# Kernel tuning notes

Measured on AMD Instinct MI355X. Metric: run time of the kernel, lower is better.

The kernel has to match this reference:

```python
import jax, jax.numpy as jnp
import numpy as np

N, E, D, H, C = 50000, 1600000, 256, 8, 32

def setup_inputs() -> dict:
    key = jax.random.key(0)
    ks = jax.random.split(key, 7)
    feat = jax.random.normal(ks[0], (N, D), dtype=jnp.float32)
    edge_weight = jax.random.uniform(ks[1], (E,), dtype=jnp.float32)
    W_lin = jax.random.normal(ks[2], (D, H * C), dtype=jnp.float32) * (1.0 / np.sqrt(D))
    att_l = jax.random.normal(ks[3], (1, H, C), dtype=jnp.float32) * (1.0 / np.sqrt(H))
    att_r = jax.random.normal(ks[4], (1, H, C), dtype=jnp.float32) * (1.0 / np.sqrt(H))
    W_res = jax.random.normal(ks[5], (D, H * C), dtype=jnp.float32) * (1.0 / np.sqrt(D))
    edge_index = jax.random.randint(ks[6], (2, E), 0, N, dtype=jnp.int32)
    return {"feat": feat, "edge_weight": edge_weight, "W_lin": W_lin,
            "att_l": att_l, "att_r": att_r, "W_res": W_res, "edge_index": edge_index}

def reference(feat, edge_weight, W_lin, att_l, att_r, W_res, edge_index):
    n_nodes = feat.shape[0]
    h, c = att_l.shape[1], att_l.shape[2]
    src, dst = edge_index[0], edge_index[1]
    # node projection: [N, H, C]
    x = (feat @ W_lin).reshape(n_nodes, h, c)
    alpha_l = (x * att_l).sum(-1)  # [N, H]
    alpha_r = (x * att_r).sum(-1)  # [N, H]
    # per-edge scores [E, H]
    alpha = alpha_l[src] + alpha_r[dst]
    alpha = edge_weight[:, None] * alpha
    alpha = jnp.where(alpha > 0, alpha, 0.2 * alpha)  # leaky_relu(0.2)
    # segment softmax over destination nodes
    amax = jax.lax.stop_gradient(jax.ops.segment_max(alpha, dst, num_segments=n_nodes))
    ex = jnp.exp(alpha - amax[dst])
    denom = jax.ops.segment_sum(ex, dst, num_segments=n_nodes)
    coeff = ex / (denom[dst] + 1e-16)  # [E, H]
    # weighted message aggregation
    msg = x[src] * coeff[:, :, None]  # [E, H, C]
    agg = jax.ops.segment_sum(msg, dst, num_segments=n_nodes)  # [N, H, C]
    out = jax.nn.elu(agg).reshape(n_nodes, h * c)
    out = out + feat @ W_res  # residual
    return out
```

## Files before the change

kernel.cpp:

```cpp
#include <hip/hip_runtime.h>
#include <stdint.h>

#define D_DIM 256
#define NPAD  640

typedef __bf16 bf16x8 __attribute__((ext_vector_type(8)));
typedef float  f32x4  __attribute__((ext_vector_type(4)));

__device__ __forceinline__ float bf2f(unsigned short u) {
  union { unsigned int i; float f; } cv; cv.i = ((unsigned int)u) << 16; return cv.f;
}
__device__ __forceinline__ unsigned short f2bf(float f) {
  union { float f; unsigned int i; } cv; cv.f = f;
  unsigned int i = cv.i;
  unsigned int lsb = (i >> 16) & 1u;
  i += 0x7fffu + lsb;
  return (unsigned short)(i >> 16);
}
__device__ __forceinline__ void gld16(const void* gptr, void* lptr) {
  __builtin_amdgcn_global_load_lds(
      (const __attribute__((address_space(1))) unsigned int*)gptr,
      (__attribute__((address_space(3))) unsigned int*)lptr, 16, 0, 0);
}

__global__ __launch_bounds__(256) void setup_fused(
    const float* __restrict__ feat, unsigned short* __restrict__ fb,
    const float* __restrict__ W_lin, const float* __restrict__ W_res,
    const float* __restrict__ att_l, const float* __restrict__ att_r,
    unsigned short* __restrict__ Bt,
    const int* __restrict__ dst, int* __restrict__ cnt, int* __restrict__ rank,
    int nelem, int E, int nb_cvt, int nb_prep) {
  int bid = blockIdx.x, t = threadIdx.x;
  if (bid < nb_cvt) {
    int i = (bid * 256 + t) * 8;
    if (i >= nelem) return;
    float4 v0 = *(const float4*)(feat + i);
    float4 v1 = *(const float4*)(feat + i + 4);
    ushort4 a, b;
    a.x = f2bf(v0.x); a.y = f2bf(v0.y); a.z = f2bf(v0.z); a.w = f2bf(v0.w);
    b.x = f2bf(v1.x); b.y = f2bf(v1.y); b.z = f2bf(v1.z); b.w = f2bf(v1.w);
    *(ushort4*)(fb + i) = a;
    *(ushort4*)(fb + i + 4) = b;
  } else if (bid < nb_cvt + nb_prep) {
    int idx = (bid - nb_cvt) * 256 + t;
    int n = idx >> 8, k = idx & 255;
    float v = 0.f;
    if (n < 256) v = W_lin[k * 256 + n];
    else if (n < 512) v = W_res[k * 256 + (n - 256)];
    else if (n < 520) {
      int h = n - 512; float s = 0.f;
      #pragma unroll
      for (int c = 0; c < 32; ++c) s += W_lin[k * 256 + h * 32 + c] * att_l[h * 32 + c];
      v = s;
    } else if (n < 528) {
      int h = n - 520; float s = 0.f;
      #pragma unroll
      for (int c = 0; c < 32; ++c) s += W_lin[k * 256 + h * 32 + c] * att_r[h * 32 + c];
      v = s;
    }
    Bt[idx] = f2bf(v);
  } else {
    int e = (bid - nb_cvt - nb_prep) * 256 + t;
    if (e < E) rank[e] = atomicAdd(&cnt[dst[e]], 1);
  }
}

__global__ __launch_bounds__(256) void scan_partial(const int* __restrict__ cnt,
                                                    int* __restrict__ bsum, int N) {
  __shared__ int s[256];
  int t = threadIdx.x;
  int i = blockIdx.x * 256 + t;
  s[t] = (i < N) ? cnt[i] : 0;
  __syncthreads();
  for (int off = 128; off > 0; off >>= 1) {
    if (t < off) s[t] += s[t + off];
    __syncthreads();
  }
  if (t == 0) bsum[blockIdx.x] = s[0];
}

__global__ __launch_bounds__(256) void scan_top(int* __restrict__ bsum, int nb) {
  __shared__ int s[256];
  int t = threadIdx.x;
  int v = (t < nb) ? bsum[t] : 0;
  s[t] = v;
  __syncthreads();
  for (int off = 1; off < 256; off <<= 1) {
    int u = (t >= off) ? s[t - off] : 0;
    __syncthreads();
    s[t] += u;
    __syncthreads();
  }
  if (t < nb) bsum[t] = s[t] - v;
}

__global__ __launch_bounds__(256) void scan_apply(const int* __restrict__ cnt,
                                                  const int* __restrict__ bsum,
                                                  int* __restrict__ row_ptr, int N) {
  __shared__ int s[256];
  int t = threadIdx.x;
  int i = blockIdx.x * 256 + t;
  int v = (i < N) ? cnt[i] : 0;
  s[t] = v;
  __syncthreads();
  for (int off = 1; off < 256; off <<= 1) {
    int u = (t >= off) ? s[t - off] : 0;
    __syncthreads();
    s[t] += u;
    __syncthreads();
  }
  int excl = bsum[blockIdx.x] + s[t] - v;
  if (i < N) {
    row_ptr[i] = excl;
    if (i == N - 1) row_ptr[N] = excl + v;
  }
}

__global__ __launch_bounds__(256) void gemm_scatter(
    const unsigned short* __restrict__ A,
    const unsigned short* __restrict__ Bt,
    float* __restrict__ out, unsigned short* __restrict__ xbf,
    float* __restrict__ alpha_l, float* __restrict__ alpha_r, int M,
    const int* __restrict__ eidx, const float* __restrict__ ew,
    const int* __restrict__ row_ptr, const int* __restrict__ rank,
    int2* __restrict__ pairs, int E, int gemm_blocks, int gx) {
  __shared__ unsigned short As[128 * 32];
  __shared__ unsigned short Bs[128 * 32];

  if ((int)blockIdx.x >= gemm_blocks) {
    int e = ((int)blockIdx.x - gemm_blocks) * 256 + threadIdx.x;
    if (e < E) {
      int d = eidx[E + e];
      int pos = row_ptr[d] + rank[e];
      int2 p; p.x = eidx[e]; p.y = __float_as_int(ew[e]);
      pairs[pos] = p;
    }
    return;
  }

  int tid  = threadIdx.x;
  int w    = tid >> 6, lane = tid & 63;
  int bm   = ((int)blockIdx.x % gx) * 128, bn = ((int)blockIdx.x / gx) * 128;
  int wm   = (w & 1) * 64, wn = (w >> 1) * 64;
  int l16  = lane & 15, quad = lane >> 4;

  f32x4 acc[4][4] = {};

  int srow = w * 32 + (lane >> 2);
  int koff = (lane & 3) * 8;

  for (int k0 = 0; k0 < 256; k0 += 32) {
    #pragma unroll
    for (int i = 0; i < 2; ++i) {
      int r  = srow + i * 16;
      int rg = bm + r; if (rg > M - 1) rg = M - 1;
      gld16(A  + (size_t)rg * 256 + k0 + koff, &As[(w * 32 + i * 16) * 32]);
      gld16(Bt + (size_t)(bn + r) * 256 + k0 + koff, &Bs[(w * 32 + i * 16) * 32]);
    }
    __syncthreads();
    bf16x8 a[4], b[4];
    #pragma unroll
    for (int mi = 0; mi < 4; ++mi)
      a[mi] = *(const bf16x8*)&As[(wm + mi * 16 + l16) * 32 + quad * 8];
    #pragma unroll
    for (int ni = 0; ni < 4; ++ni)
      b[ni] = *(const bf16x8*)&Bs[(wn + ni * 16 + l16) * 32 + quad * 8];
    #pragma unroll
    for (int mi = 0; mi < 4; ++mi)
      #pragma unroll
      for (int ni = 0; ni < 4; ++ni)
        acc[mi][ni] = __builtin_amdgcn_mfma_f32_16x16x32_bf16(a[mi], b[ni], acc[mi][ni], 0, 0, 0);
    __syncthreads();
  }

  #pragma unroll
  for (int mi = 0; mi < 4; ++mi) {
    #pragma unroll
    for (int r = 0; r < 4; ++r) {
      int row = bm + wm + mi * 16 + quad * 4 + r;
      if (row >= M) continue;
      #pragma unroll
      for (int ni = 0; ni < 4; ++ni) {
        int n = bn + wn + ni * 16 + l16;
        float v = acc[mi][ni][r];
        if (n < 256)      xbf[(size_t)row * 256 + n] = f2bf(v);
        else if (n < 512) out[(size_t)row * 256 + (n - 256)] = v;
        else if (n < 520) alpha_l[row * 8 + (n - 512)] = v;
        else if (n < 528) alpha_r[row * 8 + (n - 520)] = v;
      }
    }
  }
}

__global__ __launch_bounds__(256) void agg_kernel(
    const int* __restrict__ row_ptr, const int2* __restrict__ pairs,
    const float* __restrict__ alpha_l, const float* __restrict__ alpha_r,
    const unsigned short* __restrict__ xbf, float* __restrict__ out, int N) {
  int node = blockIdx.x * 4 + (threadIdx.x >> 6);
  if (node >= N) return;
  int lane = threadIdx.x & 63;
  int h  = lane >> 3;
  int cb = lane << 2;

  int beg = row_ptr[node], end = row_ptr[node + 1];
  float arv = alpha_r[node * 8 + h];
  float l = 0.f;
  float ac0 = 0.f, ac1 = 0.f, ac2 = 0.f, ac3 = 0.f;

  if (beg < end) {
    int last = end - 1;
    const unsigned short* xb = xbf + cb;
    for (int jg = beg; jg < end; jg += 8) {
      int2 q[8];
      #pragma unroll
      for (int u = 0; u < 8; ++u) {
        int t = jg + u; t = (t < last) ? t : last;
        q[u] = pairs[t];
      }
      float al[8];
      #pragma unroll
      for (int u = 0; u < 8; ++u) al[u] = alpha_l[(size_t)q[u].x * 8 + h];
      ushort4 xv[8];
      #pragma unroll
      for (int u = 0; u < 8; ++u)
        xv[u] = *(const ushort4*)(xb + ((size_t)q[u].x << 8));
      #pragma unroll
      for (int u = 0; u < 8; ++u) {
        float a = __int_as_float(q[u].y) * (al[u] + arv);
        a = (a > 0.f) ? a : 0.2f * a;
        float p = __expf(a);
        p = (jg + u < end) ? p : 0.f;
        l += p;
        ac0 = fmaf(p, bf2f(xv[u].x), ac0);
        ac1 = fmaf(p, bf2f(xv[u].y), ac1);
        ac2 = fmaf(p, bf2f(xv[u].z), ac2);
        ac3 = fmaf(p, bf2f(xv[u].w), ac3);
      }
    }
  }
  float r = 1.0f / (l + 1e-16f);
  float o0 = ac0 * r, o1 = ac1 * r, o2 = ac2 * r, o3 = ac3 * r;
  o0 = (o0 > 0.f) ? o0 : expm1f(o0);
  o1 = (o1 > 0.f) ? o1 : expm1f(o1);
  o2 = (o2 > 0.f) ? o2 : expm1f(o2);
  o3 = (o3 > 0.f) ? o3 : expm1f(o3);
  float4* op = (float4*)(out + ((size_t)node << 8) + cb);
  float4 res = *op;
  res.x += o0; res.y += o1; res.z += o2; res.w += o3;
  *op = res;
}

extern "C" void kernel_launch(void* const* d_in, const int* in_sizes, int n_in,
                              void* d_out, int out_size, void* d_ws, size_t ws_size,
                              hipStream_t stream) {
  const float* feat  = (const float*)d_in[0];
  const float* ew    = (const float*)d_in[1];
  const float* W_lin = (const float*)d_in[2];
  const float* att_l = (const float*)d_in[3];
  const float* att_r = (const float*)d_in[4];
  const float* W_res = (const float*)d_in[5];
  const int*   eidx  = (const int*)d_in[6];
  float* out = (float*)d_out;

  int N = in_sizes[0] / D_DIM;
  int E = in_sizes[1];

  char* p = (char*)d_ws;
  auto alloc = [&](size_t bytes) {
    char* r = p; p += (bytes + 255) & ~(size_t)255; return r;
  };
  unsigned short* xbf  = (unsigned short*)alloc((size_t)N * 256 * 2);
  unsigned short* fb   = (unsigned short*)alloc((size_t)N * 256 * 2);
  float* alpha_l       = (float*)alloc((size_t)N * 8 * 4);
  float* alpha_r       = (float*)alloc((size_t)N * 8 * 4);
  unsigned short* Bt   = (unsigned short*)alloc((size_t)NPAD * D_DIM * 2);
  int*   row_ptr       = (int*)alloc((size_t)(N + 1) * 4);
  int*   cnt           = (int*)alloc((size_t)N * 4);
  int*   rank          = (int*)alloc((size_t)E * 4);
  int*   bsum          = (int*)alloc(1024);
  int2*  pairs_sep     = (int2*)alloc((size_t)E * 8);
  bool fused_ok = ((size_t)((char*)(pairs_sep + E) - (char*)d_ws) <= ws_size);
  int2* pairs = fused_ok ? pairs_sep : (int2*)fb;

  int nb      = (N + 255) / 256;
  int nb_cvt  = (N * 256 / 8 + 255) / 256;
  int nb_prep = NPAD * D_DIM / 256;
  int nb_hist = (E + 255) / 256;
  int gx = (N + 127) / 128;
  int gemm_blocks = gx * (NPAD / 128);

  hipMemsetAsync(cnt, 0, (size_t)N * 4, stream);

  setup_fused<<<nb_cvt + nb_prep + nb_hist, 256, 0, stream>>>(
      feat, fb, W_lin, W_res, att_l, att_r, Bt, eidx + E, cnt, rank,
      N * 256, E, nb_cvt, nb_prep);

  scan_partial<<<nb, 256, 0, stream>>>(cnt, bsum, N);
  scan_top<<<1, 256, 0, stream>>>(bsum, nb);
  scan_apply<<<nb, 256, 0, stream>>>(cnt, bsum, row_ptr, N);

  if (fused_ok) {
    gemm_scatter<<<gemm_blocks + nb_hist, 256, 0, stream>>>(
        fb, Bt, out, xbf, alpha_l, alpha_r, N,
        eidx, ew, row_ptr, rank, pairs, E, gemm_blocks, gx);
  } else {
    gemm_scatter<<<gemm_blocks, 256, 0, stream>>>(
        fb, Bt, out, xbf, alpha_l, alpha_r, N,
        eidx, ew, row_ptr, rank, pairs, 0 , gemm_blocks, gx);
    gemm_scatter<<<nb_hist, 256, 0, stream>>>(
        fb, Bt, out, xbf, alpha_l, alpha_r, N,
        eidx, ew, row_ptr, rank, pairs, E, 0 , gx);
  }

  agg_kernel<<<(N + 3) / 4, 256, 0, stream>>>(row_ptr, pairs, alpha_l, alpha_r, xbf, out, N);
}
```

Before: 419.5 us.

## Overlap edge histogram with GEMM and split scatter into its own kernel

Moves the per-edge atomic histogram out of the setup kernel and co-schedules it with the projection GEMM blocks, with each thread handling eight edges. The edge scatter into CSR order becomes a standalone kernel launched after the prefix scan, instead of running alongside the GEMM. The aggregation loop unroll also drops from 8 to 4 edges per iteration, lowering register pressure but leaving fewer gathers in flight. The net effect depends on which of the two side tasks overlaps the GEMM better and costs one extra launch.

```diff
diff --git a/kernel.cpp b/kernel.cpp
--- a/kernel.cpp
+++ b/kernel.cpp
@@ -23,13 +23,11 @@
       (__attribute__((address_space(3))) unsigned int*)lptr, 16, 0, 0);
 }
 
-__global__ __launch_bounds__(256) void setup_fused(
+__global__ __launch_bounds__(256) void setup_cvt_prep(
     const float* __restrict__ feat, unsigned short* __restrict__ fb,
     const float* __restrict__ W_lin, const float* __restrict__ W_res,
     const float* __restrict__ att_l, const float* __restrict__ att_r,
-    unsigned short* __restrict__ Bt,
-    const int* __restrict__ dst, int* __restrict__ cnt, int* __restrict__ rank,
-    int nelem, int E, int nb_cvt, int nb_prep) {
+    unsigned short* __restrict__ Bt, int nelem, int nb_cvt) {
   int bid = blockIdx.x, t = threadIdx.x;
   if (bid < nb_cvt) {
     int i = (bid * 256 + t) * 8;
@@ -41,7 +39,7 @@
     b.x = f2bf(v1.x); b.y = f2bf(v1.y); b.z = f2bf(v1.z); b.w = f2bf(v1.w);
     *(ushort4*)(fb + i) = a;
     *(ushort4*)(fb + i + 4) = b;
-  } else if (bid < nb_cvt + nb_prep) {
+  } else {
     int idx = (bid - nb_cvt) * 256 + t;
     int n = idx >> 8, k = idx & 255;
     float v = 0.f;
@@ -59,9 +57,6 @@
       v = s;
     }
     Bt[idx] = f2bf(v);
-  } else {
-    int e = (bid - nb_cvt - nb_prep) * 256 + t;
-    if (e < E) rank[e] = atomicAdd(&cnt[dst[e]], 1);
   }
 }
 
@@ -116,31 +111,30 @@
   }
 }
 
-__global__ __launch_bounds__(256) void gemm_scatter(
+__global__ __launch_bounds__(256) void gemm_hist(
     const unsigned short* __restrict__ A,
     const unsigned short* __restrict__ Bt,
     float* __restrict__ out, unsigned short* __restrict__ xbf,
     float* __restrict__ alpha_l, float* __restrict__ alpha_r, int M,
-    const int* __restrict__ eidx, const float* __restrict__ ew,
-    const int* __restrict__ row_ptr, const int* __restrict__ rank,
-    int2* __restrict__ pairs, int E, int gemm_blocks, int gx) {
+    const int* __restrict__ dst, int* __restrict__ cnt, int* __restrict__ rank,
+    int E, int nb_hist, int gx) {
   __shared__ unsigned short As[128 * 32];
   __shared__ unsigned short Bs[128 * 32];
 
-  if ((int)blockIdx.x >= gemm_blocks) {
-    int e = ((int)blockIdx.x - gemm_blocks) * 256 + threadIdx.x;
-    if (e < E) {
-      int d = eidx[E + e];
-      int pos = row_ptr[d] + rank[e];
-      int2 p; p.x = eidx[e]; p.y = __float_as_int(ew[e]);
-      pairs[pos] = p;
+  if ((int)blockIdx.x < nb_hist) {
+    int base = (int)blockIdx.x * 2048 + threadIdx.x;
+    #pragma unroll
+    for (int u = 0; u < 8; ++u) {
+      int e = base + u * 256;
+      if (e < E) rank[e] = atomicAdd(&cnt[dst[e]], 1);
     }
     return;
   }
 
   int tid  = threadIdx.x;
   int w    = tid >> 6, lane = tid & 63;
-  int bm   = ((int)blockIdx.x % gx) * 128, bn = ((int)blockIdx.x / gx) * 128;
+  int gb   = (int)blockIdx.x - nb_hist;
+  int bm   = (gb % gx) * 128, bn = (gb / gx) * 128;
   int wm   = (w & 1) * 64, wn = (w >> 1) * 64;
   int l16  = lane & 15, quad = lane >> 4;
 
@@ -189,6 +183,19 @@
         else if (n < 528) alpha_r[row * 8 + (n - 520)] = v;
       }
     }
+  }
+}
+
+__global__ __launch_bounds__(256) void scatter_kernel(
+    const int* __restrict__ eidx, const float* __restrict__ ew,
+    const int* __restrict__ row_ptr, const int* __restrict__ rank,
+    int2* __restrict__ pairs, int E) {
+  int e = blockIdx.x * 256 + threadIdx.x;
+  if (e < E) {
+    int d = eidx[E + e];
+    int pos = row_ptr[d] + rank[e];
+    int2 p; p.x = eidx[e]; p.y = __float_as_int(ew[e]);
+    pairs[pos] = p;
   }
 }
 
@@ -210,22 +217,22 @@
   if (beg < end) {
     int last = end - 1;
     const unsigned short* xb = xbf + cb;
-    for (int jg = beg; jg < end; jg += 8) {
-      int2 q[8];
-      #pragma unroll
-      for (int u = 0; u < 8; ++u) {
+    for (int jg = beg; jg < end; jg += 4) {
+      int2 q[4];
+      #pragma unroll
+      for (int u = 0; u < 4; ++u) {
         int t = jg + u; t = (t < last) ? t : last;
         q[u] = pairs[t];
       }
-      float al[8];
-      #pragma unroll
-      for (int u = 0; u < 8; ++u) al[u] = alpha_l[(size_t)q[u].x * 8 + h];
-      ushort4 xv[8];
-      #pragma unroll
-      for (int u = 0; u < 8; ++u)
+      float al[4];
+      #pragma unroll
+      for (int u = 0; u < 4; ++u) al[u] = alpha_l[(size_t)q[u].x * 8 + h];
+      ushort4 xv[4];
+      #pragma unroll
+      for (int u = 0; u < 4; ++u)
         xv[u] = *(const ushort4*)(xb + ((size_t)q[u].x << 8));
       #pragma unroll
-      for (int u = 0; u < 8; ++u) {
+      for (int u = 0; u < 4; ++u) {
         float a = __int_as_float(q[u].y) * (al[u] + arv);
         a = (a > 0.f) ? a : 0.2f * a;
         float p = __expf(a);
@@ -279,38 +286,31 @@
   int*   rank          = (int*)alloc((size_t)E * 4);
   int*   bsum          = (int*)alloc(1024);
   int2*  pairs_sep     = (int2*)alloc((size_t)E * 8);
-  bool fused_ok = ((size_t)((char*)(pairs_sep + E) - (char*)d_ws) <= ws_size);
-  int2* pairs = fused_ok ? pairs_sep : (int2*)fb;
+  bool sep_ok = ((size_t)((char*)(pairs_sep + E) - (char*)d_ws) <= ws_size);
+  int2* pairs = sep_ok ? pairs_sep : (int2*)fb;
 
   int nb      = (N + 255) / 256;
   int nb_cvt  = (N * 256 / 8 + 255) / 256;
   int nb_prep = NPAD * D_DIM / 256;
-  int nb_hist = (E + 255) / 256;
+  int nb_hist = (E + 2047) / 2048;
+  int nb_scat = (E + 255) / 256;
   int gx = (N + 127) / 128;
   int gemm_blocks = gx * (NPAD / 128);
 
   hipMemsetAsync(cnt, 0, (size_t)N * 4, stream);
 
-  setup_fused<<<nb_cvt + nb_prep + nb_hist, 256, 0, stream>>>(
-      feat, fb, W_lin, W_res, att_l, att_r, Bt, eidx + E, cnt, rank,
-      N * 256, E, nb_cvt, nb_prep);
+  setup_cvt_prep<<<nb_cvt + nb_prep, 256, 0, stream>>>(
+      feat, fb, W_lin, W_res, att_l, att_r, Bt, N * 256, nb_cvt);
+
+  gemm_hist<<<nb_hist + gemm_blocks, 256, 0, stream>>>(
+      fb, Bt, out, xbf, alpha_l, alpha_r, N,
+      eidx + E, cnt, rank, E, nb_hist, gx);
 
   scan_partial<<<nb, 256, 0, stream>>>(cnt, bsum, N);
   scan_top<<<1, 256, 0, stream>>>(bsum, nb);
   scan_apply<<<nb, 256, 0, stream>>>(cnt, bsum, row_ptr, N);
 
-  if (fused_ok) {
-    gemm_scatter<<<gemm_blocks + nb_hist, 256, 0, stream>>>(
-        fb, Bt, out, xbf, alpha_l, alpha_r, N,
-        eidx, ew, row_ptr, rank, pairs, E, gemm_blocks, gx);
-  } else {
-    gemm_scatter<<<gemm_blocks, 256, 0, stream>>>(
-        fb, Bt, out, xbf, alpha_l, alpha_r, N,
-        eidx, ew, row_ptr, rank, pairs, 0 , gemm_blocks, gx);
-    gemm_scatter<<<nb_hist, 256, 0, stream>>>(
-        fb, Bt, out, xbf, alpha_l, alpha_r, N,
-        eidx, ew, row_ptr, rank, pairs, E, 0 , gx);
-  }
+  scatter_kernel<<<nb_scat, 256, 0, stream>>>(eidx, ew, row_ptr, rank, pairs, E);
 
   agg_kernel<<<(N + 3) / 4, 256, 0, stream>>>(row_ptr, pairs, alpha_l, alpha_r, xbf, out, N);
 }
```

After: 413.9 us. Within noise of the previous version (-1.3%).
